# Performance work log

Measured on AMD Instinct MI355X. Metric: run time of the kernel, lower is better.

## Reference

```python
import jax, jax.numpy as jnp
import numpy as np

N = 100000
E = 3200000
NFEAT, NHID, NCLASS = 256, 128, 40


def setup_inputs() -> dict:
    key = jax.random.key(0)
    ks = jax.random.split(key, 8)
    return {
        "x": jax.random.normal(ks[0], (N, NFEAT), dtype=jnp.float32),
        "edge_src": jax.random.randint(ks[1], (E,), 0, N, dtype=jnp.int32),
        "edge_dst": jax.random.randint(ks[2], (E,), 0, N, dtype=jnp.int32),
        "edge_w": jax.random.uniform(ks[3], (E,), dtype=jnp.float32),
        "W0": jax.random.normal(ks[4], (NFEAT, NHID), dtype=jnp.float32) * (2.0 / (NFEAT + NHID)) ** 0.5,
        "b0": jax.random.normal(ks[5], (1, NHID), dtype=jnp.float32) * 0.1,
        "W1": jax.random.normal(ks[6], (NHID, NCLASS), dtype=jnp.float32) * (2.0 / (NHID + NCLASS)) ** 0.5,
        "b1": jax.random.normal(ks[7], (1, NCLASS), dtype=jnp.float32) * 0.1,
    }


def _l2_normalize(h, eps=1e-12):
    # F.normalize(x, p=2, dim=1)
    nrm = jnp.sqrt(jnp.sum(h * h, axis=1, keepdims=True))
    return h / jnp.maximum(nrm, eps)


def reference(x, edge_src, edge_dst, edge_w, W0, b0, W1, b1):
    n_nodes = x.shape[0]

    def spmm(h):  # adj @ h with edge-list sparse adjacency
        return jax.ops.segment_sum(edge_w[:, None] * h[edge_src], edge_dst, num_segments=n_nodes)

    # layer 1: GraphConvolution = spmm(x @ W) + bias (dropout is identity in eval)
    h = spmm(x @ W0) + b0
    h = _l2_normalize(h)        # atg.Z1
    h = jax.nn.relu(h)          # atg.H1
    # layer 2
    z = spmm(h @ W1) + b1       # atg.Z2
    return jax.nn.log_softmax(z, axis=1)
```

## Files before the change

kernel.cpp:

```cpp
#include <hip/hip_runtime.h>
#include <math.h>

#define NN 100000
#define NE 3200000
#define NF 256
#define NH 128
#define NC 40

#define CH 8192
#define NBLK 391
#define NBUCK 782
#define HTOT (NBUCK * NBLK)
#define HS1 ((HTOT + 511) / 512)
#define NTILE 1563

typedef unsigned int uint;
typedef short short8 __attribute__((ext_vector_type(8)));
typedef float floatx4 __attribute__((ext_vector_type(4)));

__device__ __forceinline__ float bflo(uint v) { return __uint_as_float(v << 16); }
__device__ __forceinline__ float bfhi(uint v) { return __uint_as_float(v & 0xffff0000u); }
__device__ __forceinline__ unsigned short f2bf(float f) {
    const uint u = __float_as_uint(f);
    return (unsigned short)((u + 0x7fffu + ((u >> 16) & 1u)) >> 16);
}
__device__ __forceinline__ uint pack2bf(float a, float b) {
    return (uint)f2bf(a) | ((uint)f2bf(b) << 16);
}

union ABfrag { uint u[4]; short8 s; };

__global__ __launch_bounds__(256) void prep_pack_k(const float* __restrict__ W0,
                                                   const float* __restrict__ W1,
                                                   uint4* __restrict__ W0p,
                                                   uint4* __restrict__ W1p) {
    const int idx = blockIdx.x * 256 + threadIdx.x;
    if (idx < 4096) {
        const int lane  = idx & 63;
        const int ntile = (idx >> 6) & 7;
        const int kstep = idx >> 9;
        const int n  = ntile * 16 + (lane & 15);
        const int kb = kstep * 32 + (lane >> 4) * 8;
        uint w[4];
#pragma unroll
        for (int ww = 0; ww < 4; ++ww)
            w[ww] = pack2bf(W0[(size_t)(kb + 2 * ww) * NH + n],
                            W0[(size_t)(kb + 2 * ww + 1) * NH + n]);
        W0p[idx] = make_uint4(w[0], w[1], w[2], w[3]);
    } else if (idx < 4096 + 768) {
        const int i2 = idx - 4096;
        const int lane  = i2 & 63;
        const int ntile = (i2 >> 6) % 3;
        const int kstep = (i2 >> 6) / 3;
        const int n  = ntile * 16 + (lane & 15);
        const int kb = kstep * 32 + (lane >> 4) * 8;
        uint w[4];
#pragma unroll
        for (int ww = 0; ww < 4; ++ww) {
            const float lo = (n < NC) ? W1[(size_t)(kb + 2 * ww) * NC + n] : 0.0f;
            const float hi = (n < NC) ? W1[(size_t)(kb + 2 * ww + 1) * NC + n] : 0.0f;
            w[ww] = pack2bf(lo, hi);
        }
        W1p[i2] = make_uint4(w[0], w[1], w[2], w[3]);
    }
}

__global__ __launch_bounds__(256) void gemm1_mfma(const float* __restrict__ x,
                                                  const uint4* __restrict__ W0p,
                                                  unsigned short* __restrict__ xwh) {
    __shared__ __align__(16) uint4 sB[4096];
    for (int i = threadIdx.x; i < 4096; i += 256) sB[i] = W0p[i];
    __syncthreads();

    const int wave = threadIdx.x >> 6;
    const int lane = threadIdx.x & 63;
    const int quad = lane >> 4;
    const int mcol = lane & 15;

    for (int tile = blockIdx.x; tile < NTILE; tile += 512) {
        const int row  = tile * 64 + wave * 16 + mcol;
        const int rowc = min(row, NN - 1);
        const float* xr = x + (size_t)rowc * NF + quad * 8;

        floatx4 acc[8] = {};
        float4 lo = *(const float4*)(xr);
        float4 hi = *(const float4*)(xr + 4);
#pragma unroll
        for (int ks = 0; ks < 8; ++ks) {
            ABfrag a;
            a.u[0] = pack2bf(lo.x, lo.y);
            a.u[1] = pack2bf(lo.z, lo.w);
            a.u[2] = pack2bf(hi.x, hi.y);
            a.u[3] = pack2bf(hi.z, hi.w);
            if (ks < 7) {
                lo = *(const float4*)(xr + (ks + 1) * 32);
                hi = *(const float4*)(xr + (ks + 1) * 32 + 4);
            }
#pragma unroll
            for (int nt = 0; nt < 8; ++nt) {
                ABfrag b;
                const uint4 bw = sB[(ks * 8 + nt) * 64 + lane];
                b.u[0] = bw.x; b.u[1] = bw.y; b.u[2] = bw.z; b.u[3] = bw.w;
                acc[nt] = __builtin_amdgcn_mfma_f32_16x16x32_bf16(a.s, b.s, acc[nt], 0, 0, 0);
            }
        }
        const int rowbase = tile * 64 + wave * 16 + quad * 4;
#pragma unroll
        for (int nt = 0; nt < 8; ++nt) {
#pragma unroll
            for (int r = 0; r < 4; ++r) {
                const int rr = rowbase + r;
                if (rr < NN) xwh[(size_t)rr * NH + nt * 16 + mcol] = f2bf(acc[nt][r]);
            }
        }
    }
}

__global__ __launch_bounds__(256) void p1hist_k(const int* __restrict__ edst,
                                                int* __restrict__ hmat) {
    __shared__ uint h[NBUCK];
    for (int i = threadIdx.x; i < NBUCK; i += 256) h[i] = 0;
    __syncthreads();
    const int b = blockIdx.x;
    const int e0 = b * CH, e1 = min(NE, e0 + CH);
    for (int e = e0 + threadIdx.x * 4; e + 3 < e1; e += 1024) {
        const int4 d4 = *(const int4*)(edst + e);
        atomicAdd(&h[((uint)d4.x) >> 7], 1u);
        atomicAdd(&h[((uint)d4.y) >> 7], 1u);
        atomicAdd(&h[((uint)d4.z) >> 7], 1u);
        atomicAdd(&h[((uint)d4.w) >> 7], 1u);
    }
    __syncthreads();
    for (int i = threadIdx.x; i < NBUCK; i += 256)
        hmat[(size_t)i * NBLK + b] = (int)h[i];
}

__global__ __launch_bounds__(512) void hscan1_k(int* __restrict__ hmat,
                                                int* __restrict__ partials) {
    __shared__ int s[512];
    const int t = threadIdx.x;
    const int i = blockIdx.x * 512 + t;
    const int v = (i < HTOT) ? hmat[i] : 0;
    s[t] = v;
    __syncthreads();
#pragma unroll
    for (int off = 1; off < 512; off <<= 1) {
        int a = (t >= off) ? s[t - off] : 0;
        __syncthreads();
        s[t] += a;
        __syncthreads();
    }
    if (i < HTOT) hmat[i] = s[t] - v;
    if (t == 511) partials[blockIdx.x] = s[t];
}

__global__ __launch_bounds__(1024) void hscan2_k(int* __restrict__ partials, int nb) {
    __shared__ int s[1024];
    const int t = threadIdx.x;
    const int v = (t < nb) ? partials[t] : 0;
    s[t] = v;
    __syncthreads();
#pragma unroll
    for (int off = 1; off < 1024; off <<= 1) {
        int a = (t >= off) ? s[t - off] : 0;
        __syncthreads();
        s[t] += a;
        __syncthreads();
    }
    if (t < nb) partials[t] = s[t] - v;
}

__global__ __launch_bounds__(256) void p1scat_k(const int* __restrict__ esrc,
                                                const int* __restrict__ edst,
                                                const float* __restrict__ ew,
                                                const int* __restrict__ hmat,
                                                const int* __restrict__ partials,
                                                uint2* __restrict__ ep1) {
    __shared__ uint base[NBUCK];
    const int b = blockIdx.x;
    for (int i = threadIdx.x; i < NBUCK; i += 256) {
        const int g = i * NBLK + b;
        base[i] = (uint)(hmat[g] + partials[g >> 9]);
    }
    __syncthreads();
    const int e0 = b * CH, e1 = min(NE, e0 + CH);
    for (int e = e0 + threadIdx.x; e < e1; e += 256) {
        const uint d = (uint)edst[e];
        const uint pos = atomicAdd(&base[d >> 7], 1u);
        ep1[pos] = make_uint2((uint)esrc[e] | ((d & 127u) << 17), __float_as_uint(ew[e]));
    }
}

__global__ __launch_bounds__(256) void p2_k(const int* __restrict__ hmat,
                                            const int* __restrict__ partials,
                                            const uint2* __restrict__ ep1,
                                            uint2* __restrict__ ep,
                                            int* __restrict__ rp) {
    const int bk = blockIdx.x;
    const int gb = bk * NBLK;
    const int beg = hmat[gb] + partials[gb >> 9];
    int end;
    if (bk == NBUCK - 1) end = NE;
    else { const int ge = gb + NBLK; end = hmat[ge] + partials[ge >> 9]; }
    __shared__ uint cnt[128];
    __shared__ uint st[128];
    if (threadIdx.x < 128) cnt[threadIdx.x] = 0;
    __syncthreads();
    for (int j = beg + threadIdx.x; j < end; j += 256)
        atomicAdd(&cnt[(ep1[j].x >> 17) & 127u], 1u);
    __syncthreads();
    if (threadIdx.x < 128) st[threadIdx.x] = cnt[threadIdx.x];
    __syncthreads();
#pragma unroll
    for (int off = 1; off < 128; off <<= 1) {
        uint a = 0;
        if (threadIdx.x < 128 && threadIdx.x >= off) a = st[threadIdx.x - off];
        __syncthreads();
        if (threadIdx.x < 128) st[threadIdx.x] += a;
        __syncthreads();
    }
    if (threadIdx.x < 128) {
        const uint start = st[threadIdx.x] - cnt[threadIdx.x];
        const int d = bk * 128 + threadIdx.x;
        if (d < NN) rp[d] = beg + (int)start;
        cnt[threadIdx.x] = (uint)beg + start;
    }
    if (bk == 0 && threadIdx.x == 200) rp[NN] = NE;
    __syncthreads();
    for (int j = beg + threadIdx.x; j < end; j += 256) {
        const uint2 r = ep1[j];
        const uint pos = atomicAdd(&cnt[(r.x >> 17) & 127u], 1u);
        ep[pos] = r;
    }
}

__global__ __launch_bounds__(256) void spmm1n_g(const int* __restrict__ rp,
                                                const uint2* __restrict__ ep,
                                                const uint* __restrict__ xwb,
                                                const float* __restrict__ b0,
                                                uint* __restrict__ h2b) {
    const int n = blockIdx.x * 4 + (threadIdx.x >> 6);
    const int t = threadIdx.x & 63;
    const int beg = __builtin_amdgcn_readfirstlane(rp[n]);
    const int end = __builtin_amdgcn_readfirstlane(rp[n + 1]);
    float a0 = 0.f, a1 = 0.f;
    int j = beg;
    for (; j + 7 < end; j += 8) {
        uint sx[8];
        float w[8];
#pragma unroll
        for (int u = 0; u < 8; ++u) {
            const uint2 e = ep[j + u];
            sx[u] = __builtin_amdgcn_readfirstlane(e.x) & 0x1FFFFu;
            w[u]  = __uint_as_float(__builtin_amdgcn_readfirstlane(e.y));
        }
        uint v[8];
#pragma unroll
        for (int u = 0; u < 8; ++u) v[u] = xwb[(size_t)sx[u] * 64 + t];
#pragma unroll
        for (int u = 0; u < 8; ++u) {
            a0 = fmaf(w[u], bflo(v[u]), a0);
            a1 = fmaf(w[u], bfhi(v[u]), a1);
        }
    }
    for (; j < end; ++j) {
        const uint2 e = ep[j];
        const uint sx = __builtin_amdgcn_readfirstlane(e.x) & 0x1FFFFu;
        const float w = __uint_as_float(__builtin_amdgcn_readfirstlane(e.y));
        const uint v = xwb[(size_t)sx * 64 + t];
        a0 = fmaf(w, bflo(v), a0); a1 = fmaf(w, bfhi(v), a1);
    }
    const float2 bb = *(const float2*)(b0 + 2 * t);
    const float v0 = a0 + bb.x, v1 = a1 + bb.y;
    float s = v0 * v0 + v1 * v1;
#pragma unroll
    for (int o = 1; o < 64; o <<= 1) s += __shfl_xor(s, o, 64);
    const float scale = 1.0f / fmaxf(sqrtf(s), 1e-12f);
    h2b[(size_t)n * 64 + t] = pack2bf(fmaxf(v0 * scale, 0.0f), fmaxf(v1 * scale, 0.0f));
}

__global__ __launch_bounds__(256) void gemm2_mfma(const uint* __restrict__ h2b,
                                                  const uint4* __restrict__ W1p,
                                                  unsigned short* __restrict__ hwh) {
    __shared__ __align__(16) uint4 sB[768];
    for (int i = threadIdx.x; i < 768; i += 256) sB[i] = W1p[i];
    __syncthreads();

    const int wave = threadIdx.x >> 6;
    const int lane = threadIdx.x & 63;
    const int quad = lane >> 4;
    const int mcol = lane & 15;
    const int row  = blockIdx.x * 64 + wave * 16 + mcol;
    const int rowc = min(row, NN - 1);
    const uint* hr = h2b + (size_t)rowc * 64;

    floatx4 acc[3] = {};
#pragma unroll
    for (int ks = 0; ks < 4; ++ks) {
        ABfrag a;
        const uint4 hv = *(const uint4*)(hr + ks * 16 + quad * 4);
        a.u[0] = hv.x; a.u[1] = hv.y; a.u[2] = hv.z; a.u[3] = hv.w;
#pragma unroll
        for (int nt = 0; nt < 3; ++nt) {
            ABfrag b;
            const uint4 bw = sB[(ks * 3 + nt) * 64 + lane];
            b.u[0] = bw.x; b.u[1] = bw.y; b.u[2] = bw.z; b.u[3] = bw.w;
            acc[nt] = __builtin_amdgcn_mfma_f32_16x16x32_bf16(a.s, b.s, acc[nt], 0, 0, 0);
        }
    }
    const int rowbase = blockIdx.x * 64 + wave * 16 + quad * 4;
#pragma unroll
    for (int nt = 0; nt < 3; ++nt) {
        const int f = nt * 16 + mcol;
        if (f < NC) {
#pragma unroll
            for (int r = 0; r < 4; ++r) {
                const int rr = rowbase + r;
                if (rr < NN) hwh[(size_t)rr * NC + f] = f2bf(acc[nt][r]);
            }
        }
    }
}

__global__ __launch_bounds__(320) void spmm2l_g(const int* __restrict__ rp,
                                                const uint2* __restrict__ ep,
                                                const uint* __restrict__ hwb,
                                                const float* __restrict__ b1,
                                                float2* __restrict__ out2) {
    const int nl = threadIdx.x / 20;
    const int g  = threadIdx.x % 20;
    const int n  = blockIdx.x * 16 + nl;
    const int beg = rp[n], end = rp[n + 1];
    float a0 = 0.f, a1 = 0.f;
    int j = beg;
    for (; j + 7 < end; j += 8) {
        uint2 e[8];
        uint v[8];
#pragma unroll
        for (int u = 0; u < 8; ++u) e[u] = ep[j + u];
#pragma unroll
        for (int u = 0; u < 8; ++u) v[u] = hwb[(size_t)(e[u].x & 0x1FFFFu) * 20 + g];
#pragma unroll
        for (int u = 0; u < 8; ++u) {
            const float w = __uint_as_float(e[u].y);
            a0 = fmaf(w, bflo(v[u]), a0);
            a1 = fmaf(w, bfhi(v[u]), a1);
        }
    }
    for (; j < end; ++j) {
        const uint2 e = ep[j];
        const uint v = hwb[(size_t)(e.x & 0x1FFFFu) * 20 + g];
        const float w = __uint_as_float(e.y);
        a0 = fmaf(w, bflo(v), a0); a1 = fmaf(w, bfhi(v), a1);
    }
    const float2 bb = *(const float2*)(b1 + 2 * g);
    a0 += bb.x; a1 += bb.y;
    __shared__ float red[16 * 20];
    __shared__ float stat[16];
    red[nl * 20 + g] = fmaxf(a0, a1);
    __syncthreads();
    if (g == 0) {
        float m = -INFINITY;
#pragma unroll
        for (int q = 0; q < 20; ++q) m = fmaxf(m, red[nl * 20 + q]);
        stat[nl] = m;
    }
    __syncthreads();
    const float m = stat[nl];
    red[nl * 20 + g] = expf(a0 - m) + expf(a1 - m);
    __syncthreads();
    if (g == 0) {
        float ssum = 0.f;
#pragma unroll
        for (int q = 0; q < 20; ++q) ssum += red[nl * 20 + q];
        stat[nl] = logf(ssum);
    }
    __syncthreads();
    const float lse = stat[nl];
    out2[(size_t)n * 20 + g] = make_float2(a0 - m - lse, a1 - m - lse);
}

extern "C" void kernel_launch(void* const* d_in, const int* in_sizes, int n_in,
                              void* d_out, int out_size, void* d_ws, size_t ws_size,
                              hipStream_t stream) {
    const float* x    = (const float*)d_in[0];
    const int*   esrc = (const int*)d_in[1];
    const int*   edst = (const int*)d_in[2];
    const float* ew   = (const float*)d_in[3];
    const float* W0   = (const float*)d_in[4];
    const float* b0   = (const float*)d_in[5];
    const float* W1   = (const float*)d_in[6];
    const float* b1   = (const float*)d_in[7];
    float* out = (float*)d_out;

    size_t o = 0;
    uint*  xwb  = (uint*)d_ws + o;  o += (size_t)NN * 64;
    uint*  h2b  = (uint*)d_ws + o;  o += (size_t)NN * 64;
    uint2* ep1  = (uint2*)h2b;
    uint*  hwb  = (uint*)d_ws + o;  o += (size_t)NN * 20;
    uint2* ep   = (uint2*)((uint*)d_ws + o); o += (size_t)NE * 2;
    int*   hmat = (int*)d_ws + o;   o += HTOT;
    int*   rp   = (int*)d_ws + o;   o += NN + 2;
    int*   partials = (int*)d_ws + o; o += 1024;
    if (o & 3) o += 4 - (o & 3);
    uint4* W0p  = (uint4*)((uint*)d_ws + o); o += 16384;
    uint4* W1p  = (uint4*)((uint*)d_ws + o); o += 3072;

    prep_pack_k<<<19, 256, 0, stream>>>(W0, W1, W0p, W1p);
    gemm1_mfma<<<512, 256, 0, stream>>>(x, W0p, (unsigned short*)xwb);

    p1hist_k<<<NBLK, 256, 0, stream>>>(edst, hmat);
    hscan1_k<<<HS1, 512, 0, stream>>>(hmat, partials);
    hscan2_k<<<1, 1024, 0, stream>>>(partials, HS1);
    p1scat_k<<<NBLK, 256, 0, stream>>>(esrc, edst, ew, hmat, partials, ep1);
    p2_k<<<NBUCK, 256, 0, stream>>>(hmat, partials, ep1, ep, rp);

    spmm1n_g<<<NN / 4, 256, 0, stream>>>(rp, ep, xwb, b0, h2b);
    gemm2_mfma<<<NTILE, 256, 0, stream>>>(h2b, W1p, (unsigned short*)hwb);
    spmm2l_g<<<NN / 16, 320, 0, stream>>>(rp, ep, hwb, b1, (float2*)out);
}
```

Baseline: 512.2 us.

## Pad layer-2 features to 32 lanes, shuffle-based softmax, prefetch edge batches

The hidden-by-W1 intermediate is now stored padded to 64 bf16 per row (128-byte aligned rows), and gemm2 zero-fills the padding. The second SpMM maps each node to a 32-lane group, so the log-softmax reductions use warp shuffles instead of shared-memory passes and block barriers. Both SpMM kernels software-pipeline the next batch of 8 edge records while the current gathers are consumed. The padding enlarges the intermediate buffer and gather footprint, and 12 of the 32 lanes per node stay idle.

```diff
diff --git a/kernel.cpp b/kernel.cpp
--- a/kernel.cpp
+++ b/kernel.cpp
@@ -13,6 +13,7 @@
 #define HTOT (NBUCK * NBLK)
 #define HS1 ((HTOT + 511) / 512)
 #define NTILE 1563
+#define NCP 32
 
 typedef unsigned int uint;
 typedef short short8 __attribute__((ext_vector_type(8)));
@@ -245,22 +246,34 @@
     const int end = __builtin_amdgcn_readfirstlane(rp[n + 1]);
     float a0 = 0.f, a1 = 0.f;
     int j = beg;
-    for (; j + 7 < end; j += 8) {
-        uint sx[8];
-        float w[8];
-#pragma unroll
-        for (int u = 0; u < 8; ++u) {
-            const uint2 e = ep[j + u];
-            sx[u] = __builtin_amdgcn_readfirstlane(e.x) & 0x1FFFFu;
-            w[u]  = __uint_as_float(__builtin_amdgcn_readfirstlane(e.y));
-        }
-        uint v[8];
-#pragma unroll
-        for (int u = 0; u < 8; ++u) v[u] = xwb[(size_t)sx[u] * 64 + t];
-#pragma unroll
-        for (int u = 0; u < 8; ++u) {
-            a0 = fmaf(w[u], bflo(v[u]), a0);
-            a1 = fmaf(w[u], bfhi(v[u]), a1);
+    const int e8 = end - 7;
+    if (j < e8) {
+        uint2 e[8];
+#pragma unroll
+        for (int u = 0; u < 8; ++u) e[u] = ep[j + u];
+        for (;;) {
+            uint sx[8];
+            float w[8];
+#pragma unroll
+            for (int u = 0; u < 8; ++u) {
+                sx[u] = __builtin_amdgcn_readfirstlane(e[u].x) & 0x1FFFFu;
+                w[u]  = __uint_as_float(__builtin_amdgcn_readfirstlane(e[u].y));
+            }
+            uint v[8];
+#pragma unroll
+            for (int u = 0; u < 8; ++u) v[u] = xwb[(size_t)sx[u] * 64 + t];
+            j += 8;
+            const bool more = (j < e8);
+            if (more) {
+#pragma unroll
+                for (int u = 0; u < 8; ++u) e[u] = ep[j + u];
+            }
+#pragma unroll
+            for (int u = 0; u < 8; ++u) {
+                a0 = fmaf(w[u], bflo(v[u]), a0);
+                a1 = fmaf(w[u], bfhi(v[u]), a1);
+            }
+            if (!more) break;
         }
     }
     for (; j < end; ++j) {
@@ -312,72 +325,74 @@
 #pragma unroll
     for (int nt = 0; nt < 3; ++nt) {
         const int f = nt * 16 + mcol;
-        if (f < NC) {
-#pragma unroll
-            for (int r = 0; r < 4; ++r) {
-                const int rr = rowbase + r;
-                if (rr < NN) hwh[(size_t)rr * NC + f] = f2bf(acc[nt][r]);
-            }
-        }
-    }
-}
-
-__global__ __launch_bounds__(320) void spmm2l_g(const int* __restrict__ rp,
+#pragma unroll
+        for (int r = 0; r < 4; ++r) {
+            const int rr = rowbase + r;
+            if (rr < NN)
+                hwh[(size_t)rr * (2 * NCP) + f] = (f < NC) ? f2bf(acc[nt][r]) : (unsigned short)0;
+        }
+    }
+#pragma unroll
+    for (int r = 0; r < 4; ++r) {
+        const int rr = rowbase + r;
+        if (rr < NN) hwh[(size_t)rr * (2 * NCP) + 48 + mcol] = (unsigned short)0;
+    }
+}
+
+__global__ __launch_bounds__(256) void spmm2l_g(const int* __restrict__ rp,
                                                 const uint2* __restrict__ ep,
                                                 const uint* __restrict__ hwb,
                                                 const float* __restrict__ b1,
                                                 float2* __restrict__ out2) {
-    const int nl = threadIdx.x / 20;
-    const int g  = threadIdx.x % 20;
-    const int n  = blockIdx.x * 16 + nl;
+    const int n = blockIdx.x * 8 + (threadIdx.x >> 5);
+    const int g = threadIdx.x & 31;
     const int beg = rp[n], end = rp[n + 1];
     float a0 = 0.f, a1 = 0.f;
     int j = beg;
-    for (; j + 7 < end; j += 8) {
+    const int e8 = end - 7;
+    if (j < e8) {
         uint2 e[8];
-        uint v[8];
 #pragma unroll
         for (int u = 0; u < 8; ++u) e[u] = ep[j + u];
-#pragma unroll
-        for (int u = 0; u < 8; ++u) v[u] = hwb[(size_t)(e[u].x & 0x1FFFFu) * 20 + g];
-#pragma unroll
-        for (int u = 0; u < 8; ++u) {
-            const float w = __uint_as_float(e[u].y);
-            a0 = fmaf(w, bflo(v[u]), a0);
-            a1 = fmaf(w, bfhi(v[u]), a1);
+        for (;;) {
+            uint v[8];
+#pragma unroll
+            for (int u = 0; u < 8; ++u)
+                v[u] = hwb[(size_t)(e[u].x & 0x1FFFFu) * NCP + g];
+            float w[8];
+#pragma unroll
+            for (int u = 0; u < 8; ++u) w[u] = __uint_as_float(e[u].y);
+            j += 8;
+            const bool more = (j < e8);
+            if (more) {
+#pragma unroll
+                for (int u = 0; u < 8; ++u) e[u] = ep[j + u];
+            }
+#pragma unroll
+            for (int u = 0; u < 8; ++u) {
+                a0 = fmaf(w[u], bflo(v[u]), a0);
+                a1 = fmaf(w[u], bfhi(v[u]), a1);
+            }
+            if (!more) break;
         }
     }
     for (; j < end; ++j) {
         const uint2 e = ep[j];
-        const uint v = hwb[(size_t)(e.x & 0x1FFFFu) * 20 + g];
+        const uint v = hwb[(size_t)(e.x & 0x1FFFFu) * NCP + g];
         const float w = __uint_as_float(e.y);
         a0 = fmaf(w, bflo(v), a0); a1 = fmaf(w, bfhi(v), a1);
     }
-    const float2 bb = *(const float2*)(b1 + 2 * g);
-    a0 += bb.x; a1 += bb.y;
-    __shared__ float red[16 * 20];
-    __shared__ float stat[16];
-    red[nl * 20 + g] = fmaxf(a0, a1);
-    __syncthreads();
-    if (g == 0) {
-        float m = -INFINITY;
-#pragma unroll
-        for (int q = 0; q < 20; ++q) m = fmaxf(m, red[nl * 20 + q]);
-        stat[nl] = m;
-    }
-    __syncthreads();
-    const float m = stat[nl];
-    red[nl * 20 + g] = expf(a0 - m) + expf(a1 - m);
-    __syncthreads();
-    if (g == 0) {
-        float ssum = 0.f;
-#pragma unroll
-        for (int q = 0; q < 20; ++q) ssum += red[nl * 20 + q];
-        stat[nl] = logf(ssum);
-    }
-    __syncthreads();
-    const float lse = stat[nl];
-    out2[(size_t)n * 20 + g] = make_float2(a0 - m - lse, a1 - m - lse);
+    float bb0 = 0.f, bb1 = 0.f;
+    if (g < 20) { const float2 bb = *(const float2*)(b1 + 2 * g); bb0 = bb.x; bb1 = bb.y; }
+    a0 += bb0; a1 += bb1;
+    float m = (g < 20) ? fmaxf(a0, a1) : -INFINITY;
+#pragma unroll
+    for (int o = 1; o < 32; o <<= 1) m = fmaxf(m, __shfl_xor(m, o, 32));
+    float s = (g < 20) ? (expf(a0 - m) + expf(a1 - m)) : 0.f;
+#pragma unroll
+    for (int o = 1; o < 32; o <<= 1) s += __shfl_xor(s, o, 32);
+    const float lse = logf(s);
+    if (g < 20) out2[(size_t)n * 20 + g] = make_float2(a0 - m - lse, a1 - m - lse);
 }
 
 extern "C" void kernel_launch(void* const* d_in, const int* in_sizes, int n_in,
@@ -397,7 +412,7 @@
     uint*  xwb  = (uint*)d_ws + o;  o += (size_t)NN * 64;
     uint*  h2b  = (uint*)d_ws + o;  o += (size_t)NN * 64;
     uint2* ep1  = (uint2*)h2b;
-    uint*  hwb  = (uint*)d_ws + o;  o += (size_t)NN * 20;
+    uint*  hwb  = (uint*)d_ws + o;  o += (size_t)NN * NCP;
     uint2* ep   = (uint2*)((uint*)d_ws + o); o += (size_t)NE * 2;
     int*   hmat = (int*)d_ws + o;   o += HTOT;
     int*   rp   = (int*)d_ws + o;   o += NN + 2;
@@ -417,5 +432,5 @@
 
     spmm1n_g<<<NN / 4, 256, 0, stream>>>(rp, ep, xwb, b0, h2b);
     gemm2_mfma<<<NTILE, 256, 0, stream>>>(h2b, W1p, (unsigned short*)hwb);
-    spmm2l_g<<<NN / 16, 320, 0, stream>>>(rp, ep, hwb, b1, (float2*)out);
-}
+    spmm2l_g<<<NN / 8, 256, 0, stream>>>(rp, ep, hwb, b1, (float2*)out);
+}
```

Measured after the change: 506.3 us. Within noise of the previous version (-1.2%).
